# Optimization experiments

Measured on AMD Instinct MI355X. Metric: run time of the kernel, lower is better.

The kernel has to match this reference:

```python
import jax, jax.numpy as jnp
import numpy as np

N = 50000
E = 1600000
NUM_GRAPHS = 64
NEG_SLOPE = 0.2


def _glorot(key, shape):
    fan_in, fan_out = shape[0], shape[-1]
    lim = jnp.sqrt(6.0 / (fan_in + fan_out))
    return jax.random.uniform(key, shape, jnp.float32, -lim, lim)


def setup_inputs() -> dict:
    key = jax.random.key(0)
    ks = jax.random.split(key, 16)
    x = jax.random.normal(ks[0], (N, 128), jnp.float32)
    edge_index = jax.random.randint(ks[1], (2, E), 0, N, jnp.int64)
    batch = jnp.sort(jax.random.randint(ks[2], (N,), 0, NUM_GRAPHS, jnp.int64))
    dims = [(128, 32), (32, 64), (64, 128)]
    params = {}
    for i, (fi, fo) in enumerate(dims, start=1):
        params[f'W{i}'] = _glorot(ks[3 * i], (fi, fo))
        params[f'a_src{i}'] = _glorot(ks[3 * i + 1], (1, fo))[0]
        params[f'a_dst{i}'] = _glorot(ks[3 * i + 2], (1, fo))[0]
        params[f'b{i}'] = jnp.zeros((fo,), jnp.float32)
    params['lin1_W'] = _glorot(ks[12], (128, 32))
    params['lin1_b'] = jnp.zeros((32,), jnp.float32)
    params['lin2_W'] = _glorot(ks[13], (32, 10))
    params['lin2_b'] = jnp.zeros((10,), jnp.float32)
    return dict(x=x, edge_index=edge_index, batch=batch, **params)


def gat_conv(x, src, dst, W, a_src, a_dst, b):
    # h: [N, F_out]
    h = x @ W
    # per-node attention logits, gathered per edge
    as_n = h @ a_src  # [N]
    ad_n = h @ a_dst  # [N]
    e = jax.nn.leaky_relu(as_n[src] + ad_n[dst], NEG_SLOPE)  # [E']
    # segment softmax over incoming edges of each destination node
    m = jax.ops.segment_max(e, dst, num_segments=N)
    ee = jnp.exp(e - m[dst])
    s = jax.ops.segment_sum(ee, dst, num_segments=N)
    alpha = ee / (s[dst] + 1e-16)
    # weighted scatter-add of source messages
    out = jax.ops.segment_sum(h[src] * alpha[:, None], dst, num_segments=N)
    return out + b


def reference(x, edge_index, batch, W1, a_src1, a_dst1, b1, W2, a_src2, a_dst2, b2,
              W3, a_src3, a_dst3, b3, lin1_W, lin1_b, lin2_W, lin2_b):
    # add self loops (PyG GATConv default)
    loops = jnp.arange(N, dtype=edge_index.dtype)
    src = jnp.concatenate([edge_index[0], loops])
    dst = jnp.concatenate([edge_index[1], loops])
    h = jax.nn.relu(gat_conv(x, src, dst, W1, a_src1, a_dst1, b1))
    h = jax.nn.relu(gat_conv(h, src, dst, W2, a_src2, a_dst2, b2))
    h = gat_conv(h, src, dst, W3, a_src3, a_dst3, b3)
    # global_add_pool over graphs
    g = jax.ops.segment_sum(h, batch, num_segments=NUM_GRAPHS)  # [G, 128]
    g = jax.nn.relu(g @ lin1_W + lin1_b)
    g = g @ lin2_W + lin2_b
    # faithful to original: log_softmax over dim=0 (batch axis)
    return jax.nn.log_softmax(g, axis=0)
```

## Files before the change

kernel.cpp:

```cpp
#include <hip/hip_runtime.h>
#include <cstdint>
#include <cstddef>

#define NN 50000
#define NE 1600000
#define NG 64
#define NCB 391
#define HB 98
#define EPB_A 8192
#define CAP_B 8192

__device__ __forceinline__ float bflo(unsigned u) { return __uint_as_float(u << 16); }
__device__ __forceinline__ float bfhi(unsigned u) { return __uint_as_float(u & 0xffff0000u); }
__device__ __forceinline__ unsigned f2bf(float f) {
    unsigned u = __float_as_uint(f);
    return (u + 0x7fffu + ((u >> 16) & 1u)) >> 16;
}
__device__ __forceinline__ float rdlane_f(float v, int l) {
    return __uint_as_float((unsigned)__builtin_amdgcn_readlane((int)__float_as_uint(v), l));
}

template <int FIN, int FOUT, bool HIST>
__global__ void gemm_att_k(const float* __restrict__ A, const float* __restrict__ W,
                           const float* __restrict__ a_src, const float* __restrict__ a_dst,
                           unsigned* __restrict__ Hb, float* __restrict__ as_,
                           float* __restrict__ ad_, int gemmBlocks,
                           const int* __restrict__ edst, int* __restrict__ gcount) {
    __shared__ float Wl[FIN * FOUT];
    __shared__ float Al[32 * FIN];
    __shared__ int hh[NCB];
    int tid = threadIdx.x;
    if (HIST && blockIdx.x >= gemmBlocks) {
        int bid = blockIdx.x - gemmBlocks;
        for (int i = tid; i < NCB; i += 256) hh[i] = 0;
        __syncthreads();
        const int total4 = NE / 4;
        for (int i = bid * 256 + tid; i < total4; i += HB * 256) {
            int4 d = ((const int4*)edst)[i];
            atomicAdd(&hh[d.x >> 7], 1);
            atomicAdd(&hh[d.y >> 7], 1);
            atomicAdd(&hh[d.z >> 7], 1);
            atomicAdd(&hh[d.w >> 7], 1);
        }
        __syncthreads();
        for (int i = tid; i < NCB; i += 256)
            if (hh[i]) atomicAdd(&gcount[i], hh[i]);
        return;
    }
    const int RPB = 32;
    const int CP = FOUT / 2;
    const int CLANES = 256 / CP;
    const int RL = RPB / CLANES;
    for (int i = tid; i < (FIN * FOUT) / 4; i += 256)
        ((float4*)Wl)[i] = ((const float4*)W)[i];
    int rowbase = blockIdx.x * RPB;
    int nrows = min(RPB, NN - rowbase);
    int nel4 = (nrows * FIN) / 4;
    const float4* Asrc = (const float4*)(A + (size_t)rowbase * FIN);
    for (int i = tid; i < nel4; i += 256) ((float4*)Al)[i] = Asrc[i];
    __syncthreads();
    int c2 = tid % CP;
    int rb = tid / CP;
    float acc0[RL], acc1[RL];
#pragma unroll
    for (int r = 0; r < RL; ++r) { acc0[r] = 0.f; acc1[r] = 0.f; }
#pragma unroll 4
    for (int k = 0; k < FIN; ++k) {
        float w0 = Wl[k * FOUT + 2 * c2];
        float w1 = Wl[k * FOUT + 2 * c2 + 1];
#pragma unroll
        for (int r = 0; r < RL; ++r) {
            float a = Al[(rb + r * CLANES) * FIN + k];
            acc0[r] += a * w0;
            acc1[r] += a * w1;
        }
    }
    float2 asrc2 = ((const float2*)a_src)[c2];
    float2 adst2 = ((const float2*)a_dst)[c2];
#pragma unroll
    for (int r = 0; r < RL; ++r) {
        int row = rowbase + rb + r * CLANES;
        float p1 = acc0[r] * asrc2.x + acc1[r] * asrc2.y;
        float p2 = acc0[r] * adst2.x + acc1[r] * adst2.y;
#pragma unroll
        for (int o = CP >> 1; o; o >>= 1) {
            p1 += __shfl_xor(p1, o, CP);
            p2 += __shfl_xor(p2, o, CP);
        }
        if (row < NN) {
            Hb[(size_t)row * CP + c2] = f2bf(acc0[r]) | (f2bf(acc1[r]) << 16);
            if (c2 == 0) { as_[row] = p1; ad_[row] = p2; }
        }
    }
}

__global__ void cscan_k(const int* __restrict__ gcount, int* __restrict__ cbase,
                        int* __restrict__ gcur) {
    __shared__ int part[256];
    int tid = threadIdx.x;
    int i0 = 2 * tid, i1 = 2 * tid + 1;
    int v0 = (i0 < NCB) ? gcount[i0] : 0;
    int v1 = (i1 < NCB) ? gcount[i1] : 0;
    part[tid] = v0 + v1;
    __syncthreads();
    for (int off = 1; off < 256; off <<= 1) {
        int v = (tid >= off) ? part[tid - off] : 0;
        __syncthreads();
        part[tid] += v;
        __syncthreads();
    }
    int run = tid ? part[tid - 1] : 0;
    if (i0 < NCB) { cbase[i0] = run; gcur[i0] = run; run += v0; }
    if (i1 < NCB) { cbase[i1] = run; gcur[i1] = run; run += v1; }
    if (tid == 255) cbase[NCB] = part[255];
}

__global__ void parta_k(const int* __restrict__ esrc, const int* __restrict__ edst,
                        int* __restrict__ gcur, int* __restrict__ pk_g) {
    __shared__ int cnt[NCB];
    __shared__ int base[NCB];
    __shared__ int cur[NCB];
    __shared__ int gposs[NCB];
    __shared__ int sc[256];
    __shared__ int lpk[EPB_A];
    int tid = threadIdx.x;
    int e0 = blockIdx.x * EPB_A;
    int e1 = min(e0 + EPB_A, NE);
    for (int i = tid; i < NCB; i += 256) cnt[i] = 0;
    __syncthreads();
    for (int i = e0 / 4 + tid; i < e1 / 4; i += 256) {
        int4 d = ((const int4*)edst)[i];
        atomicAdd(&cnt[d.x >> 7], 1);
        atomicAdd(&cnt[d.y >> 7], 1);
        atomicAdd(&cnt[d.z >> 7], 1);
        atomicAdd(&cnt[d.w >> 7], 1);
    }
    __syncthreads();
    int i0 = 2 * tid, i1 = 2 * tid + 1;
    int c0 = (i0 < NCB) ? cnt[i0] : 0;
    int c1 = (i1 < NCB) ? cnt[i1] : 0;
    sc[tid] = c0 + c1;
    __syncthreads();
    for (int off = 1; off < 256; off <<= 1) {
        int v = (tid >= off) ? sc[tid - off] : 0;
        __syncthreads();
        sc[tid] += v;
        __syncthreads();
    }
    int run = tid ? sc[tid - 1] : 0;
    if (i0 < NCB) {
        base[i0] = run; cur[i0] = run;
        gposs[i0] = atomicAdd(&gcur[i0], c0);
        run += c0;
    }
    if (i1 < NCB) {
        base[i1] = run; cur[i1] = run;
        gposs[i1] = atomicAdd(&gcur[i1], c1);
        run += c1;
    }
    __syncthreads();
    for (int i = e0 / 4 + tid; i < e1 / 4; i += 256) {
        int4 d = ((const int4*)edst)[i];
        int4 s = ((const int4*)esrc)[i];
        lpk[atomicAdd(&cur[d.x >> 7], 1)] = s.x | ((d.x & 127) << 17);
        lpk[atomicAdd(&cur[d.y >> 7], 1)] = s.y | ((d.y & 127) << 17);
        lpk[atomicAdd(&cur[d.z >> 7], 1)] = s.z | ((d.z & 127) << 17);
        lpk[atomicAdd(&cur[d.w >> 7], 1)] = s.w | ((d.w & 127) << 17);
    }
    __syncthreads();
    int wid = tid >> 6, lane = tid & 63;
    for (int c = wid; c < NCB; c += 4) {
        int n = cnt[c], gb = gposs[c], lb = base[c];
        for (int i = lane; i < n; i += 64) pk_g[gb + i] = lpk[lb + i];
    }
}

__global__ void partb_k(const int* __restrict__ pk_g, const int* __restrict__ cbase,
                        int* __restrict__ offsets, int* __restrict__ csr) {
    __shared__ int cnt[128];
    __shared__ int sc[256];
    __shared__ int lpk[CAP_B];
    int b = blockIdx.x, tid = threadIdx.x;
    int ebeg = cbase[b], eend = cbase[b + 1], n = eend - ebeg;
    int nbeg = b * 128;
    int ncnt = min(128, NN - nbeg);
    if (tid < 128) cnt[tid] = 0;
    __syncthreads();
    bool fits = (n <= CAP_B);
    if (fits) {
        for (int i = tid; i < n; i += 256) {
            int p = pk_g[ebeg + i];
            lpk[i] = p;
            atomicAdd(&cnt[p >> 17], 1);
        }
    } else {
        for (int i = tid; i < n; i += 256) atomicAdd(&cnt[pk_g[ebeg + i] >> 17], 1);
    }
    __syncthreads();
    int c0 = (tid < 128) ? cnt[tid] : 0;
    sc[tid] = c0;
    __syncthreads();
    for (int off = 1; off < 128; off <<= 1) {
        int v = (tid >= off && tid < 128) ? sc[tid - off] : 0;
        __syncthreads();
        if (tid < 128) sc[tid] += v;
        __syncthreads();
    }
    int excl = (tid < 128) ? sc[tid] - c0 : 0;
    if (tid < ncnt) offsets[nbeg + tid] = ebeg + excl;
    if (b == NCB - 1 && tid == 0) offsets[NN] = eend;
    __syncthreads();
    if (tid < 128) cnt[tid] = ebeg + excl;
    __syncthreads();
    if (fits) {
        for (int i = tid; i < n; i += 256) {
            int p = lpk[i];
            csr[atomicAdd(&cnt[p >> 17], 1)] = p & 0x1FFFF;
        }
    } else {
        for (int i = tid; i < n; i += 256) {
            int p = pk_g[ebeg + i];
            csr[atomicAdd(&cnt[p >> 17], 1)] = p & 0x1FFFF;
        }
    }
}

template <int F, bool RELU>
__global__ void node_agg_k(const int* __restrict__ off, const int* __restrict__ csr,
                           const float* __restrict__ as_, const float* __restrict__ ad_,
                           const unsigned* __restrict__ Hb2,
                           const float* __restrict__ b, float* __restrict__ O) {
    int lane = threadIdx.x;
    int node = blockIdx.x;
    int beg = off[node], end = off[node + 1];
    float adn = ad_[node];
    float vself = as_[node] + adn;
    vself = vself > 0.f ? vself : 0.2f * vself;
    float eself = __expf(vself);
    float lsum = 0.f;

    if constexpr (F == 128) {
        unsigned hbs = Hb2[(size_t)node * 64 + lane];
        float accx = eself * bflo(hbs);
        float accy = eself * bfhi(hbs);
        for (int i0 = beg; i0 < end; i0 += 64) {
            int idx = i0 + lane;
            bool ok = idx < end;
            int s = ok ? csr[idx] : 0;
            float v = as_[s] + adn;
            v = v > 0.f ? v : 0.2f * v;
            float ee = ok ? __expf(v) : 0.f;
            lsum += ee;
            int rem = min(end - i0, 64);
            int j = 0;
            for (; j + 16 <= rem; j += 16) {
#pragma unroll
                for (int k = 0; k < 16; ++k) {
                    int s2 = __builtin_amdgcn_readlane(s, j + k);
                    float ee2 = rdlane_f(ee, j + k);
                    unsigned hb = (Hb2 + (size_t)s2 * 64)[lane];
                    accx += ee2 * bflo(hb);
                    accy += ee2 * bfhi(hb);
                }
            }
            for (; j + 4 <= rem; j += 4) {
#pragma unroll
                for (int k = 0; k < 4; ++k) {
                    int s2 = __builtin_amdgcn_readlane(s, j + k);
                    float ee2 = rdlane_f(ee, j + k);
                    unsigned hb = (Hb2 + (size_t)s2 * 64)[lane];
                    accx += ee2 * bflo(hb);
                    accy += ee2 * bfhi(hb);
                }
            }
            for (; j < rem; ++j) {
                int s2 = __builtin_amdgcn_readlane(s, j);
                float ee2 = rdlane_f(ee, j);
                unsigned hb = (Hb2 + (size_t)s2 * 64)[lane];
                accx += ee2 * bflo(hb);
                accy += ee2 * bfhi(hb);
            }
        }
#pragma unroll
        for (int o = 32; o; o >>= 1) lsum += __shfl_xor(lsum, o);
        float inv = 1.f / (lsum + eself + 1e-16f);
        float2 bb = ((const float2*)b)[lane];
        float ox = accx * inv + bb.x;
        float oy = accy * inv + bb.y;
        if (RELU) { ox = fmaxf(ox, 0.f); oy = fmaxf(oy, 0.f); }
        ((float2*)O)[(size_t)node * 64 + lane] = make_float2(ox, oy);
    } else if constexpr (F == 64) {
        int sg = lane >> 5;
        int cl = lane & 31;
        unsigned hbs = Hb2[(size_t)node * 32 + cl];
        float accx = (sg == 0) ? eself * bflo(hbs) : 0.f;
        float accy = (sg == 0) ? eself * bfhi(hbs) : 0.f;
        for (int i0 = beg; i0 < end; i0 += 64) {
            int idx = i0 + lane;
            bool ok = idx < end;
            int s = ok ? csr[idx] : 0;
            float v = as_[s] + adn;
            v = v > 0.f ? v : 0.2f * v;
            float ee = ok ? __expf(v) : 0.f;
            lsum += ee;
            int rem = min(end - i0, 64);
            int nj = (rem + 1) >> 1;
            nj = (nj + 3) & ~3;
            for (int j = 0; j < nj; j += 4) {
#pragma unroll
                for (int k = 0; k < 4; ++k) {
                    int pos = (j + k) * 2 + sg;
                    int s2 = __shfl(s, pos);
                    float ee2 = __shfl(ee, pos);
                    unsigned hb = Hb2[(size_t)s2 * 32 + cl];
                    accx += ee2 * bflo(hb);
                    accy += ee2 * bfhi(hb);
                }
            }
        }
#pragma unroll
        for (int o = 32; o; o >>= 1) lsum += __shfl_xor(lsum, o);
        float sum = lsum + eself;
        accx += __shfl_xor(accx, 32);
        accy += __shfl_xor(accy, 32);
        if (sg == 0) {
            float inv = 1.f / (sum + 1e-16f);
            float2 bb = ((const float2*)b)[cl];
            float ox = accx * inv + bb.x;
            float oy = accy * inv + bb.y;
            if (RELU) { ox = fmaxf(ox, 0.f); oy = fmaxf(oy, 0.f); }
            ((float2*)O)[(size_t)node * 32 + cl] = make_float2(ox, oy);
        }
    } else {
        const int GRP = 16, EPG = 4, U = 4;
        int sg = lane / GRP;
        int cl = lane % GRP;
        unsigned hbs = Hb2[(size_t)node * GRP + cl];
        float accx = (sg == 0) ? eself * bflo(hbs) : 0.f;
        float accy = (sg == 0) ? eself * bfhi(hbs) : 0.f;
        for (int i0 = beg; i0 < end; i0 += 64) {
            int idx = i0 + lane;
            bool ok = idx < end;
            int s = ok ? csr[idx] : 0;
            float v = as_[s] + adn;
            v = v > 0.f ? v : 0.2f * v;
            float ee = ok ? __expf(v) : 0.f;
            lsum += ee;
            int rem = min(end - i0, 64);
            int nj = (rem + EPG - 1) / EPG;
            nj = (nj + U - 1) & ~(U - 1);
            for (int j = 0; j < nj; j += U) {
#pragma unroll
                for (int k = 0; k < U; ++k) {
                    int pos = (j + k) * EPG + sg;
                    int s2 = __shfl(s, pos);
                    float ee2 = __shfl(ee, pos);
                    unsigned hb = Hb2[(size_t)s2 * GRP + cl];
                    accx += ee2 * bflo(hb);
                    accy += ee2 * bfhi(hb);
                }
            }
        }
#pragma unroll
        for (int o = 32; o; o >>= 1) lsum += __shfl_xor(lsum, o);
        float sum = lsum + eself;
#pragma unroll
        for (int o = 32; o >= GRP; o >>= 1) {
            accx += __shfl_xor(accx, o);
            accy += __shfl_xor(accy, o);
        }
        if (sg == 0) {
            float inv = 1.f / (sum + 1e-16f);
            float2 bb = ((const float2*)b)[cl];
            float ox = accx * inv + bb.x;
            float oy = accy * inv + bb.y;
            if (RELU) { ox = fmaxf(ox, 0.f); oy = fmaxf(oy, 0.f); }
            ((float2*)O)[(size_t)node * GRP + cl] = make_float2(ox, oy);
        }
    }
}

__global__ void pool_k(const float* __restrict__ O, const int* __restrict__ batch,
                       float* __restrict__ g, int nodes_per_block) {
    __shared__ float acc[NG * 128];
    int c = threadIdx.x;
    for (int i = 0; i < NG; ++i) acc[i * 128 + c] = 0.f;
    int start = blockIdx.x * nodes_per_block;
    int end = min(start + nodes_per_block, NN);
    int gmin = NG - 1, gmax = 0;
    for (int nd = start; nd < end; ++nd) {
        int gg = batch[nd];
        gmin = min(gmin, gg);
        gmax = max(gmax, gg);
        acc[gg * 128 + c] += O[(size_t)nd * 128 + c];
    }
    for (int i = gmin; i <= gmax; ++i) atomicAdd(g + i * 128 + c, acc[i * 128 + c]);
}

__global__ void head_k(const float* __restrict__ g, const float* __restrict__ l1W,
                       const float* __restrict__ l1b, const float* __restrict__ l2W,
                       const float* __restrict__ l2b, float* __restrict__ out) {
    __shared__ float h1[NG * 32];
    __shared__ float o[NG * 10];
    int tid = threadIdx.x;
    for (int idx = tid; idx < NG * 32; idx += 256) {
        int r = idx / 32, c = idx % 32;
        float acc = l1b[c];
        for (int k = 0; k < 128; ++k) acc += g[r * 128 + k] * l1W[k * 32 + c];
        h1[idx] = fmaxf(acc, 0.f);
    }
    __syncthreads();
    for (int idx = tid; idx < NG * 10; idx += 256) {
        int r = idx / 10, c = idx % 10;
        float acc = l2b[c];
        for (int k = 0; k < 32; ++k) acc += h1[r * 32 + k] * l2W[k * 10 + c];
        o[idx] = acc;
    }
    __syncthreads();
    if (tid < 10) {
        float mx = -1e30f;
        for (int r = 0; r < NG; ++r) mx = fmaxf(mx, o[r * 10 + tid]);
        float sum = 0.f;
        for (int r = 0; r < NG; ++r) sum += __expf(o[r * 10 + tid] - mx);
        float lse = mx + logf(sum);
        for (int r = 0; r < NG; ++r) out[r * 10 + tid] = o[r * 10 + tid] - lse;
    }
}

extern "C" void kernel_launch(void* const* d_in, const int* in_sizes, int n_in,
                              void* d_out, int out_size, void* d_ws, size_t ws_size,
                              hipStream_t stream) {
    const float* x   = (const float*)d_in[0];
    const int* ei    = (const int*)d_in[1];
    const int* batch = (const int*)d_in[2];
    const float* W1 = (const float*)d_in[3];
    const float* as1 = (const float*)d_in[4];
    const float* ad1 = (const float*)d_in[5];
    const float* b1 = (const float*)d_in[6];
    const float* W2 = (const float*)d_in[7];
    const float* as2 = (const float*)d_in[8];
    const float* ad2 = (const float*)d_in[9];
    const float* b2 = (const float*)d_in[10];
    const float* W3 = (const float*)d_in[11];
    const float* as3 = (const float*)d_in[12];
    const float* ad3 = (const float*)d_in[13];
    const float* b3 = (const float*)d_in[14];
    const float* l1W = (const float*)d_in[15];
    const float* l1b = (const float*)d_in[16];
    const float* l2W = (const float*)d_in[17];
    const float* l2b = (const float*)d_in[18];
    float* out = (float*)d_out;

    const int* esrc = ei;
    const int* edst = ei + NE;

    char* ws = (char*)d_ws;
    float* B0 = (float*)ws;
    float* B1 = B0 + (size_t)NN * 128;
    unsigned* Hb = (unsigned*)(B1 + (size_t)NN * 64);
    float* as_ = (float*)(Hb + (size_t)NN * 64);
    float* ad_ = as_ + NN;
    int* gcount = (int*)(ad_ + NN);
    float* g    = (float*)(gcount + NCB);
    int* cbase  = (int*)(g + NG * 128);
    int* gcur   = cbase + NCB + 1;
    int* offsets = gcur + NCB + 2;
    int* csr    = offsets + NN + 1;
    int* pk     = csr + NE;
    const int GEMM_BLOCKS = (NN + 31) / 32;

    hipMemsetAsync(gcount, 0, (NCB + NG * 128) * 4, stream);

    gemm_att_k<128, 32, true><<<GEMM_BLOCKS + HB, 256, 0, stream>>>(
        x, W1, as1, ad1, Hb, as_, ad_, GEMM_BLOCKS, edst, gcount);
    cscan_k<<<1, 256, 0, stream>>>(gcount, cbase, gcur);
    parta_k<<<(NE + EPB_A - 1) / EPB_A, 256, 0, stream>>>(esrc, edst, gcur, pk);
    partb_k<<<NCB, 256, 0, stream>>>(pk, cbase, offsets, csr);
    node_agg_k<32, true><<<NN, 64, 0, stream>>>(offsets, csr, as_, ad_, Hb, b1, B0);

    gemm_att_k<32, 64, false><<<GEMM_BLOCKS, 256, 0, stream>>>(
        B0, W2, as2, ad2, Hb, as_, ad_, GEMM_BLOCKS, nullptr, nullptr);
    node_agg_k<64, true><<<NN, 64, 0, stream>>>(offsets, csr, as_, ad_, Hb, b2, B1);

    gemm_att_k<64, 128, false><<<GEMM_BLOCKS, 256, 0, stream>>>(
        B1, W3, as3, ad3, Hb, as_, ad_, GEMM_BLOCKS, nullptr, nullptr);
    node_agg_k<128, false><<<NN, 64, 0, stream>>>(offsets, csr, as_, ad_, Hb, b3, B0);

    pool_k<<<(NN + 127) / 128, 128, 0, stream>>>(B0, batch, g, 128);
    head_k<<<1, 256, 0, stream>>>(g, l1W, l1b, l2W, l2b, out);
}
```

Baseline: 289.0 us.

## Store intermediate activations as bf16 and fuse graph pooling into last aggregation

Layer 1 and 2 aggregation outputs are written as packed bf16 and unpacked to fp32 when the next GEMM loads them, halving that traffic. The final aggregation atomically adds each node's output directly into the per-graph pooled buffer, removing the fp32 output write and the separate pool kernel. The risk is heavy global atomic contention on a small 64x128 buffer, plus bf16 rounding of intermediate activations.

```diff
diff --git a/kernel.cpp b/kernel.cpp
--- a/kernel.cpp
+++ b/kernel.cpp
@@ -20,8 +20,8 @@
     return __uint_as_float((unsigned)__builtin_amdgcn_readlane((int)__float_as_uint(v), l));
 }
 
-template <int FIN, int FOUT, bool HIST>
-__global__ void gemm_att_k(const float* __restrict__ A, const float* __restrict__ W,
+template <int FIN, int FOUT, bool HIST, bool ABF16>
+__global__ void gemm_att_k(const void* __restrict__ Ain, const float* __restrict__ W,
                            const float* __restrict__ a_src, const float* __restrict__ a_dst,
                            unsigned* __restrict__ Hb, float* __restrict__ as_,
                            float* __restrict__ ad_, int gemmBlocks,
@@ -56,8 +56,17 @@
     int rowbase = blockIdx.x * RPB;
     int nrows = min(RPB, NN - rowbase);
     int nel4 = (nrows * FIN) / 4;
-    const float4* Asrc = (const float4*)(A + (size_t)rowbase * FIN);
-    for (int i = tid; i < nel4; i += 256) ((float4*)Al)[i] = Asrc[i];
+    if (ABF16) {
+        const ushort4* As = (const ushort4*)Ain + (size_t)rowbase * (FIN / 4);
+        for (int i = tid; i < nel4; i += 256) {
+            ushort4 u = As[i];
+            ((float4*)Al)[i] = make_float4(bflo((unsigned)u.x), bflo((unsigned)u.y),
+                                           bflo((unsigned)u.z), bflo((unsigned)u.w));
+        }
+    } else {
+        const float4* As = (const float4*)Ain + (size_t)rowbase * (FIN / 4);
+        for (int i = tid; i < nel4; i += 256) ((float4*)Al)[i] = As[i];
+    }
     __syncthreads();
     int c2 = tid % CP;
     int rb = tid / CP;
@@ -225,11 +234,12 @@
     }
 }
 
-template <int F, bool RELU>
+template <int F, bool RELU, bool POOL>
 __global__ void node_agg_k(const int* __restrict__ off, const int* __restrict__ csr,
                            const float* __restrict__ as_, const float* __restrict__ ad_,
                            const unsigned* __restrict__ Hb2,
-                           const float* __restrict__ b, float* __restrict__ O) {
+                           const float* __restrict__ b, unsigned* __restrict__ Ob,
+                           const int* __restrict__ batch, float* __restrict__ g) {
     int lane = threadIdx.x;
     int node = blockIdx.x;
     int beg = off[node], end = off[node + 1];
@@ -288,7 +298,13 @@
         float ox = accx * inv + bb.x;
         float oy = accy * inv + bb.y;
         if (RELU) { ox = fmaxf(ox, 0.f); oy = fmaxf(oy, 0.f); }
-        ((float2*)O)[(size_t)node * 64 + lane] = make_float2(ox, oy);
+        if (POOL) {
+            int gg = batch[node];
+            atomicAdd(&g[gg * 128 + 2 * lane], ox);
+            atomicAdd(&g[gg * 128 + 2 * lane + 1], oy);
+        } else {
+            Ob[(size_t)node * 64 + lane] = f2bf(ox) | (f2bf(oy) << 16);
+        }
     } else if constexpr (F == 64) {
         int sg = lane >> 5;
         int cl = lane & 31;
@@ -329,7 +345,7 @@
             float ox = accx * inv + bb.x;
             float oy = accy * inv + bb.y;
             if (RELU) { ox = fmaxf(ox, 0.f); oy = fmaxf(oy, 0.f); }
-            ((float2*)O)[(size_t)node * 32 + cl] = make_float2(ox, oy);
+            Ob[(size_t)node * 32 + cl] = f2bf(ox) | (f2bf(oy) << 16);
         }
     } else {
         const int GRP = 16, EPG = 4, U = 4;
@@ -375,26 +391,9 @@
             float ox = accx * inv + bb.x;
             float oy = accy * inv + bb.y;
             if (RELU) { ox = fmaxf(ox, 0.f); oy = fmaxf(oy, 0.f); }
-            ((float2*)O)[(size_t)node * GRP + cl] = make_float2(ox, oy);
-        }
-    }
-}
-
-__global__ void pool_k(const float* __restrict__ O, const int* __restrict__ batch,
-                       float* __restrict__ g, int nodes_per_block) {
-    __shared__ float acc[NG * 128];
-    int c = threadIdx.x;
-    for (int i = 0; i < NG; ++i) acc[i * 128 + c] = 0.f;
-    int start = blockIdx.x * nodes_per_block;
-    int end = min(start + nodes_per_block, NN);
-    int gmin = NG - 1, gmax = 0;
-    for (int nd = start; nd < end; ++nd) {
-        int gg = batch[nd];
-        gmin = min(gmin, gg);
-        gmax = max(gmax, gg);
-        acc[gg * 128 + c] += O[(size_t)nd * 128 + c];
-    }
-    for (int i = gmin; i <= gmax; ++i) atomicAdd(g + i * 128 + c, acc[i * 128 + c]);
+            Ob[(size_t)node * GRP + cl] = f2bf(ox) | (f2bf(oy) << 16);
+        }
+    }
 }
 
 __global__ void head_k(const float* __restrict__ g, const float* __restrict__ l1W,
@@ -455,10 +454,10 @@
     const int* edst = ei + NE;
 
     char* ws = (char*)d_ws;
-    float* B0 = (float*)ws;
-    float* B1 = B0 + (size_t)NN * 128;
-    unsigned* Hb = (unsigned*)(B1 + (size_t)NN * 64);
-    float* as_ = (float*)(Hb + (size_t)NN * 64);
+    unsigned* Hb  = (unsigned*)ws;
+    unsigned* B0b = Hb + (size_t)NN * 64;
+    unsigned* B1b = B0b + (size_t)NN * 16;
+    float* as_ = (float*)(B1b + (size_t)NN * 32);
     float* ad_ = as_ + NN;
     int* gcount = (int*)(ad_ + NN);
     float* g    = (float*)(gcount + NCB);
@@ -471,21 +470,23 @@
 
     hipMemsetAsync(gcount, 0, (NCB + NG * 128) * 4, stream);
 
-    gemm_att_k<128, 32, true><<<GEMM_BLOCKS + HB, 256, 0, stream>>>(
+    gemm_att_k<128, 32, true, false><<<GEMM_BLOCKS + HB, 256, 0, stream>>>(
         x, W1, as1, ad1, Hb, as_, ad_, GEMM_BLOCKS, edst, gcount);
     cscan_k<<<1, 256, 0, stream>>>(gcount, cbase, gcur);
     parta_k<<<(NE + EPB_A - 1) / EPB_A, 256, 0, stream>>>(esrc, edst, gcur, pk);
     partb_k<<<NCB, 256, 0, stream>>>(pk, cbase, offsets, csr);
-    node_agg_k<32, true><<<NN, 64, 0, stream>>>(offsets, csr, as_, ad_, Hb, b1, B0);
-
-    gemm_att_k<32, 64, false><<<GEMM_BLOCKS, 256, 0, stream>>>(
-        B0, W2, as2, ad2, Hb, as_, ad_, GEMM_BLOCKS, nullptr, nullptr);
-    node_agg_k<64, true><<<NN, 64, 0, stream>>>(offsets, csr, as_, ad_, Hb, b2, B1);
-
-    gemm_att_k<64, 128, false><<<GEMM_BLOCKS, 256, 0, stream>>>(
-        B1, W3, as3, ad3, Hb, as_, ad_, GEMM_BLOCKS, nullptr, nullptr);
-    node_agg_k<128, false><<<NN, 64, 0, stream>>>(offsets, csr, as_, ad_, Hb, b3, B0);
-
-    pool_k<<<(NN + 127) / 128, 128, 0, stream>>>(B0, batch, g, 128);
+    node_agg_k<32, true, false><<<NN, 64, 0, stream>>>(offsets, csr, as_, ad_, Hb, b1,
+                                                       B0b, nullptr, nullptr);
+
+    gemm_att_k<32, 64, false, true><<<GEMM_BLOCKS, 256, 0, stream>>>(
+        B0b, W2, as2, ad2, Hb, as_, ad_, GEMM_BLOCKS, nullptr, nullptr);
+    node_agg_k<64, true, false><<<NN, 64, 0, stream>>>(offsets, csr, as_, ad_, Hb, b2,
+                                                       B1b, nullptr, nullptr);
+
+    gemm_att_k<64, 128, false, true><<<GEMM_BLOCKS, 256, 0, stream>>>(
+        B1b, W3, as3, ad3, Hb, as_, ad_, GEMM_BLOCKS, nullptr, nullptr);
+    node_agg_k<128, false, true><<<NN, 64, 0, stream>>>(offsets, csr, as_, ad_, Hb, b3,
+                                                        nullptr, batch, g);
+
     head_k<<<1, 256, 0, stream>>>(g, l1W, l1b, l2W, l2b, out);
 }
```

Result: slower. 416.1 us (+44.0%).
